# Kernel tuning notes

Hardware: AMD Instinct MI355X
Metric: run time of the kernel (lower is better)

Reference implementation:

```python
import jax, jax.numpy as jnp
import numpy as np
import math

D = 6       # input_size (raw particle features)
H = 128     # hidden_size
B, N, T = 128, 64, 64  # batch, objects, timesteps (T <= max_len 100)


def setup_inputs() -> dict:
    key = jax.random.key(0)
    ks = jax.random.split(key, 16)
    def lin(k, fan_in, shape):
        return (jax.random.uniform(k, shape, jnp.float32) * 2.0 - 1.0) / np.sqrt(fan_in)
    dm = D + H  # 134, PE / readout feature dim
    return {
        "x": jax.random.normal(ks[0], (B, N, T, D), jnp.float32),
        # particle_embedding Linear(D, H)
        "W_emb": lin(ks[1], D, (D, H)), "b_emb": lin(ks[2], D, (H,)),
        # GRU(H, H): torch layout (3H, in)
        "W_ih": lin(ks[3], H, (3 * H, H)), "W_hh": lin(ks[4], H, (3 * H, H)),
        "b_ih": lin(ks[5], H, (3 * H,)), "b_hh": lin(ks[6], H, (3 * H,)),
        # gate_nn: Linear(dm,H) -> SiLU -> Linear(H,1)
        "Wg1": lin(ks[7], dm, (dm, H)), "bg1": lin(ks[8], dm, (H,)),
        "Wg2": lin(ks[9], H, (H, 1)), "bg2": lin(ks[10], H, (1,)),
        # nn: Linear(dm,H) -> SiLU -> Linear(H,H)
        "Wn1": lin(ks[11], dm, (dm, H)), "bn1": lin(ks[12], dm, (H,)),
        "Wn2": lin(ks[13], H, (H, H)), "bn2": lin(ks[14], H, (H,)),
    }


def _positional_encoding(seq_len, d_model, dtype):
    pos = jnp.arange(seq_len, dtype=dtype)[:, None]                      # [T,1]
    div = jnp.exp(jnp.arange(0, d_model, 2, dtype=dtype) * (-math.log(10000.0) / d_model))
    ang = pos * div                                                       # [T, dm/2]
    # interleave sin (even idx) and cos (odd idx)
    return jnp.stack([jnp.sin(ang), jnp.cos(ang)], axis=-1).reshape(seq_len, d_model)


def _gru_last_hidden(y, W_ih, W_hh, b_ih, b_hh):
    # y: [BN, T, H]; PyTorch GRU gate order: r, z, n
    BN, Tn, Hh = y.shape
    xp = y @ W_ih.T + b_ih                       # [BN, T, 3H], input projections
    def step(h, xp_t):
        gh = h @ W_hh.T + b_hh                   # [BN, 3H]
        xr, xz, xn = jnp.split(xp_t, 3, axis=-1)
        hr, hz, hn = jnp.split(gh, 3, axis=-1)
        r = jax.nn.sigmoid(xr + hr)
        z = jax.nn.sigmoid(xz + hz)
        n = jnp.tanh(xn + r * hn)
        h_new = (1.0 - z) * n + z * h
        return h_new, None
    h0 = jnp.zeros((BN, Hh), y.dtype)
    h_last, _ = jax.lax.scan(step, h0, jnp.swapaxes(xp, 0, 1))
    return h_last                                 # [BN, H]


def reference(x, W_emb, b_emb, W_ih, W_hh, b_ih, b_hh,
              Wg1, bg1, Wg2, bg2, Wn1, bn1, Wn2, bn2):
    Bb, Nn, Tt, Dd = x.shape
    Hh = W_emb.shape[1]
    dm = Dd + Hh
    # particle embedding + GRU over time per (batch, object)
    y = (x @ W_emb + b_emb).reshape(Bb * Nn, Tt, Hh)
    h = _gru_last_hidden(y, W_ih, W_hh, b_ih, b_hh)       # [B*N, H]
    # broadcast last hidden state over timesteps, concat with raw positions
    h_exp = jnp.broadcast_to(h[:, None, :], (Bb * Nn, Tt, Hh))
    aug = jnp.concatenate([x.reshape(Bb * Nn, Tt, Dd), h_exp], axis=-1)  # [B*N, T, dm]
    aug = aug + _positional_encoding(Tt, dm, x.dtype)      # PE (dropout in eval = identity)
    feats = aug.reshape(Bb * Nn * Tt, dm)                  # [M, dm]
    # AttentionalAggregation: segment softmax over batch index
    seg = jnp.repeat(jnp.arange(Bb), Nn * Tt)              # [M]
    gate = jax.nn.silu(feats @ Wg1 + bg1) @ Wg2 + bg2      # [M, 1]
    gate = gate[:, 0]
    val = jax.nn.silu(feats @ Wn1 + bn1) @ Wn2 + bn2       # [M, H]
    gmax = jax.ops.segment_max(gate, seg, num_segments=Bb)
    e = jnp.exp(gate - gmax[seg])
    denom = jax.ops.segment_sum(e, seg, num_segments=Bb)
    w = e / denom[seg]                                      # [M]
    out = jax.ops.segment_sum(w[:, None] * val, seg, num_segments=Bb)  # [B, H]
    return out
```

## Files before the change

### kernel.cpp

```cpp
#include <hip/hip_runtime.h>

using bf8v = __bf16 __attribute__((ext_vector_type(8)));
using s4v  = short  __attribute__((ext_vector_type(4)));
using f4v  = float  __attribute__((ext_vector_type(4)));

#define L2E 1.44269504088896340f

__device__ __forceinline__ float ex2(float x){ float r; asm("v_exp_f32 %0, %1" : "=v"(r) : "v"(x)); return r; }
__device__ __forceinline__ float rcp_(float x){ float r; asm("v_rcp_f32 %0, %1" : "=v"(r) : "v"(x)); return r; }
__device__ __forceinline__ float sigm(float x){ return rcp_(1.0f + ex2(-L2E*x)); }
__device__ __forceinline__ float tanh_(float x){ return 1.0f - 2.0f*rcp_(1.0f + ex2(2.0f*L2E*x)); }
__device__ __forceinline__ short f2bf(float x){ return __builtin_bit_cast(short, (__bf16)x); }
__device__ __forceinline__ f4v splat4(float v){ f4v r = {v,v,v,v}; return r; }
__device__ __forceinline__ f4v mfma16(bf8v a, bf8v b, f4v c){
  return __builtin_amdgcn_mfma_f32_16x16x32_bf16(a, b, c, 0, 0, 0);
}

__global__ void prep_kernel(
    const float* __restrict__ W_emb, const float* __restrict__ b_emb,
    const float* __restrict__ W_ih,  const float* __restrict__ W_hh,
    const float* __restrict__ b_ih,
    const float* __restrict__ Wg1,   const float* __restrict__ Wn1,
    const float* __restrict__ Wn2,
    const float* __restrict__ bg1,   const float* __restrict__ bn1,
    short* __restrict__ bhhf, short* __restrict__ wcf, short* __restrict__ wn2f,
    short* __restrict__ w2f, float* __restrict__ b2, float* __restrict__ pe,
    float* __restrict__ bc)
{
  int i = blockIdx.x*256 + threadIdx.x;
  if (i < 49152){
    int e = i&7, lane=(i>>3)&63, r=i>>9; int nt=r%24, kb=r/24;
    int k = kb*32 + ((lane>>4)<<3) + e;
    int n = nt*16 + (lane&15);
    bhhf[i] = f2bf(W_hh[n*128 + k]);
    return;
  }
  i -= 49152;
  if (i < 40960){
    int e=i&7, lane=(i>>3)&63, r=i>>9; int nt=r%16, kb=r/16;
    int k = kb*32 + ((lane>>4)<<3) + e; int n = nt*16 + (lane&15);
    float v = 0.f;
    if (k < 134) v = (n < 128) ? Wg1[k*128 + n] : Wn1[k*128 + (n-128)];
    wcf[i] = f2bf(v);
    return;
  }
  i -= 40960;
  if (i < 16384){
    int e=i&7, lane=(i>>3)&63, r=i>>9; int nt=r%8, kb=r/8;
    int k = kb*32 + ((lane>>4)<<3) + e; int n = nt*16 + (lane&15);
    wn2f[i] = f2bf(Wn2[k*128 + n]);
    return;
  }
  i -= 16384;
  if (i < 12288){
    int e=i&7, lane=(i>>3)&63, nt=i>>9;
    int k = ((lane>>4)<<3) + e; int n = nt*16 + (lane&15);
    float v = 0.f;
    if (k < 6){
      const float* we = W_emb + k*128; const float* wi = W_ih + n*128;
      float s = 0.f;
      for (int h2=0; h2<128; ++h2) s += we[h2]*wi[h2];
      v = s;
    }
    w2f[i] = f2bf(v);
    return;
  }
  i -= 12288;
  if (i < 384){
    float s = b_ih[i]; const float* wi = W_ih + i*128;
    for (int h2=0; h2<128; ++h2) s += b_emb[h2]*wi[h2];
    b2[i] = s;
    return;
  }
  i -= 384;
  if (i < 10240){
    int t = i/160, k = i%160;
    float v = 0.f;
    if (k < 134){
      float fr = expf(-(float)(k & ~1) * 9.210340371976184f / 134.f);
      float a = (float)t * fr;
      v = (k&1) ? cosf(a) : sinf(a);
    }
    pe[i] = v;
    return;
  }
  i -= 10240;
  if (i < 256){ bc[i] = (i < 128) ? bg1[i] : bn1[i-128]; return; }
}

__global__ __launch_bounds__(512, 2) void gru_kernel(
    const float* __restrict__ x,
    const short* __restrict__ bhhf,
    const short* __restrict__ w2f,
    const float* __restrict__ b2,
    const float* __restrict__ b_hh,
    float* __restrict__ h_out)
{
  __shared__ alignas(16) short h_lds[2][16*128];
  const int tid = threadIdx.x;
  const int w = tid >> 6;
  const int lane = tid & 63;
  const int l15 = lane & 15, lhi = lane >> 4;
  const int blk = blockIdx.x;

  for (int i = tid; i < 16*128; i += 512) h_lds[0][i] = 0;

  bf8v bhh[4][3]; bf8v w2v[3];
  float b2v[3], bhv[3];
  #pragma unroll
  for (int g = 0; g < 3; ++g){
    int nt = g*8 + w;
    w2v[g] = *reinterpret_cast<const bf8v*>(w2f + ((nt*64 + lane)<<3));
    #pragma unroll
    for (int kb = 0; kb < 4; ++kb)
      bhh[kb][g] = *reinterpret_cast<const bf8v*>(bhhf + (((kb*24 + nt)*64 + lane)<<3));
    int col = nt*16 + l15;
    b2v[g] = b2[col]; bhv[g] = b_hh[col];
  }
  float hreg[4] = {0.f,0.f,0.f,0.f};
  __syncthreads();

  const float* xrow = x + (size_t)((blk*16 + l15)*64)*6;
  const int sw_r = (l15 & 7) << 4;

  float xv[6];
  #pragma unroll
  for (int j = 0; j < 6; ++j) xv[j] = xrow[j];

#define GSTEP(RD, WR, TN)                                                     \
  {                                                                           \
    bf8v ax;                                                                  \
    _Pragma("unroll")                                                         \
    for (int i2=0;i2<8;++i2) ax[i2] = (__bf16)0.f;                            \
    if (lhi == 0){                                                            \
      ax[0]=(__bf16)xv[0]; ax[1]=(__bf16)xv[1]; ax[2]=(__bf16)xv[2];          \
      ax[3]=(__bf16)xv[3]; ax[4]=(__bf16)xv[4]; ax[5]=(__bf16)xv[5];          \
    }                                                                         \
    float xn[6];                                                              \
    _Pragma("unroll")                                                         \
    for (int j2=0;j2<6;++j2) xn[j2] = xrow[(TN)*6 + j2];                      \
    bf8v ah[4];                                                               \
    _Pragma("unroll")                                                         \
    for (int kb = 0; kb < 4; ++kb){                                           \
      int off = l15*256 + ((kb*64 + lhi*16) ^ sw_r);                          \
      ah[kb] = *reinterpret_cast<const bf8v*>((const char*)(RD) + off);       \
    }                                                                         \
    f4v xpa[3], gha[3];                                                       \
    _Pragma("unroll")                                                         \
    for (int g = 0; g < 3; ++g){                                              \
      xpa[g] = splat4(b2v[g]);                                                \
      xpa[g] = mfma16(ax, w2v[g], xpa[g]);                                    \
      gha[g] = splat4(bhv[g]);                                                \
      _Pragma("unroll")                                                       \
      for (int kb = 0; kb < 4; ++kb) gha[g] = mfma16(ah[kb], bhh[kb][g], gha[g]); \
    }                                                                         \
    _Pragma("unroll")                                                         \
    for (int r = 0; r < 4; ++r){                                              \
      float rg = sigm(xpa[0][r] + gha[0][r]);                                 \
      float zg = sigm(xpa[1][r] + gha[1][r]);                                 \
      float ng = tanh_(xpa[2][r] + rg*gha[2][r]);                             \
      float hv = ng + zg*(hreg[r] - ng);                                      \
      hreg[r] = hv;                                                           \
      int s = lhi*4 + r;                                                      \
      int off = s*256 + (((w*16 + l15)*2) ^ ((s&7)<<4));                      \
      *(short*)((char*)(WR) + off) = f2bf(hv);                                \
    }                                                                         \
    _Pragma("unroll")                                                         \
    for (int j3=0;j3<6;++j3) xv[j3] = xn[j3];                                 \
    __syncthreads();                                                          \
  }

  for (int t = 0; t < 64; t += 2){
    GSTEP(h_lds[0], h_lds[1], t+1);
    GSTEP(h_lds[1], h_lds[0], (t+2 > 63 ? 63 : t+2));
  }
#undef GSTEP

  #pragma unroll
  for (int r = 0; r < 4; ++r){
    int s = lhi*4 + r;
    h_out[(size_t)(blk*16 + s)*128 + w*16 + l15] = hreg[r];
  }
}

__global__ __launch_bounds__(256, 4) void feats_kernel(
    const float* __restrict__ x, const float* __restrict__ h_out,
    const float* __restrict__ pe,
    const short* __restrict__ wcf, const short* __restrict__ wn2f,
    const float* __restrict__ bc, const float* __restrict__ Wg2,
    const float* __restrict__ bg2, const float* __restrict__ bn2,
    float* __restrict__ partials)
{
  __shared__ alignas(16) char AB[64*384];
  __shared__ alignas(16) float hb[160];
  __shared__ alignas(16) float xs[384];
  __shared__ float gp[2][64];
  __shared__ float gate_arr[64];

  const int tid = threadIdx.x;
  const int w = tid >> 6;
  const int lane = tid & 63;
  const int l15 = lane & 15, lhi = lane >> 4;
  const int seq = blockIdx.x;

  if (tid < 160) hb[tid] = (tid >= 6 && tid < 134) ? h_out[(size_t)seq*128 + tid - 6] : 0.f;
  if (tid < 96) *reinterpret_cast<f4v*>(xs + tid*4) =
      *reinterpret_cast<const f4v*>(x + (size_t)seq*384 + tid*4);
  __syncthreads();

  {
    int m = tid >> 2, q = tid & 3, k0 = q*40;
    float xr8[8] = {0.f,0.f,0.f,0.f,0.f,0.f,0.f,0.f};
    if (q == 0){
      #pragma unroll
      for (int j = 0; j < 6; ++j) xr8[j] = xs[m*6 + j];
    }
    const float* per = pe + m*160 + k0;
    const f4v* hb4 = reinterpret_cast<const f4v*>(hb + k0);
    int swm = (m & 7) << 4;
    #pragma unroll
    for (int j = 0; j < 10; ++j){
      f4v v = hb4[j];
      f4v p4 = *reinterpret_cast<const f4v*>(per + 4*j);
      v += p4;
      if (j < 2){
        v[0] += xr8[4*j+0]; v[1] += xr8[4*j+1];
        v[2] += xr8[4*j+2]; v[3] += xr8[4*j+3];
      }
      s4v o;
      #pragma unroll
      for (int c = 0; c < 4; ++c) o[c] = f2bf(v[c]);
      int off = m*384 + (((k0 + 4*j)*2) ^ swm);
      *reinterpret_cast<s4v*>(AB + off) = o;
    }
  }
  __syncthreads();

  const int ntb = w*4;
  float bcv[4];
  #pragma unroll
  for (int i=0;i<4;++i) bcv[i] = bc[(ntb+i)*16 + l15];
  f4v acc[4][4];
  #pragma unroll
  for (int mt=0;mt<4;++mt)
    #pragma unroll
    for (int i=0;i<4;++i) acc[mt][i] = splat4(bcv[i]);
  #pragma unroll
  for (int kb = 0; kb < 5; ++kb){
    bf8v a[4];
    #pragma unroll
    for (int mt=0;mt<4;++mt){
      int row = l15 + 16*mt;
      int off = row*384 + ((kb*64 + lhi*16) ^ ((row&7)<<4));
      a[mt] = *reinterpret_cast<const bf8v*>(AB + off);
    }
    bf8v b[4];
    #pragma unroll
    for (int i=0;i<4;++i)
      b[i] = *reinterpret_cast<const bf8v*>(wcf + (((kb*16 + ntb + i)*64 + lane)<<3));
    #pragma unroll
    for (int mt=0;mt<4;++mt)
      #pragma unroll
      for (int i=0;i<4;++i) acc[mt][i] = mfma16(a[mt], b[i], acc[mt][i]);
  }
  __syncthreads();

  if (w < 2){
    float wg2v[4];
    #pragma unroll
    for (int i=0;i<4;++i) wg2v[i] = Wg2[(ntb+i)*16 + l15];
    #pragma unroll
    for (int mt=0;mt<4;++mt)
      #pragma unroll
      for (int r=0;r<4;++r){
        float p = 0.f;
        #pragma unroll
        for (int i=0;i<4;++i){ float v = acc[mt][i][r]; p += v*sigm(v)*wg2v[i]; }
        p += __shfl_xor(p, 1); p += __shfl_xor(p, 2);
        p += __shfl_xor(p, 4); p += __shfl_xor(p, 8);
        if (l15 == 0) gp[w][mt*16 + lhi*4 + r] = p;
      }
  } else {
    #pragma unroll
    for (int mt=0;mt<4;++mt)
      #pragma unroll
      for (int i=0;i<4;++i)
        #pragma unroll
        for (int r=0;r<4;++r){
          float v = acc[mt][i][r]; float s = v*sigm(v);
          int row = mt*16 + lhi*4 + r;
          int colb = (((w-2)*4 + i)*16 + l15)*2;
          int off = row*256 + (colb ^ ((row&7)<<4));
          *(short*)(AB + off) = f2bf(s);
        }
  }
  __syncthreads();

  if (tid < 64) gate_arr[tid] = bg2[0] + gp[0][tid] + gp[1][tid];

  const int nt2b = w*2;
  float bn2v[2];
  #pragma unroll
  for (int i=0;i<2;++i) bn2v[i] = bn2[(nt2b+i)*16 + l15];
  f4v acc2[4][2];
  #pragma unroll
  for (int mt=0;mt<4;++mt)
    #pragma unroll
    for (int i=0;i<2;++i) acc2[mt][i] = splat4(bn2v[i]);
  #pragma unroll
  for (int kb = 0; kb < 4; ++kb){
    bf8v a2f[4];
    #pragma unroll
    for (int mt=0;mt<4;++mt){
      int row = l15 + 16*mt;
      int off = row*256 + ((kb*64 + lhi*16) ^ ((row&7)<<4));
      a2f[mt] = *reinterpret_cast<const bf8v*>(AB + off);
    }
    bf8v b2f[2];
    #pragma unroll
    for (int i=0;i<2;++i)
      b2f[i] = *reinterpret_cast<const bf8v*>(wn2f + (((kb*8 + nt2b + i)*64 + lane)<<3));
    #pragma unroll
    for (int mt=0;mt<4;++mt)
      #pragma unroll
      for (int i=0;i<2;++i) acc2[mt][i] = mfma16(a2f[mt], b2f[i], acc2[mt][i]);
  }
  __syncthreads();

  float g = gate_arr[lane];
  float M = g;
  #pragma unroll
  for (int d=1; d<64; d<<=1) M = fmaxf(M, __shfl_xor(M, d));
  float e = ex2((g - M)*L2E);
  float sE = e;
  #pragma unroll
  for (int d=1; d<64; d<<=1) sE += __shfl_xor(sE, d);
  float ev0 = 0.f, ev1 = 0.f;
  #pragma unroll
  for (int mt=0;mt<4;++mt)
    #pragma unroll
    for (int r=0;r<4;++r){
      int row = mt*16 + lhi*4 + r;
      float wm = ex2((gate_arr[row] - M)*L2E);
      ev0 += wm*acc2[mt][0][r];
      ev1 += wm*acc2[mt][1][r];
    }
  ev0 += __shfl_xor(ev0, 16); ev0 += __shfl_xor(ev0, 32);
  ev1 += __shfl_xor(ev1, 16); ev1 += __shfl_xor(ev1, 32);

  float* pb = partials + (size_t)seq*130;
  if (tid == 0){ pb[0] = M; pb[1] = sE; }
  if (lane < 16){
    pb[2 + (nt2b+0)*16 + lane] = ev0;
    pb[2 + (nt2b+1)*16 + lane] = ev1;
  }
}

__global__ void combine_kernel(const float* __restrict__ partials, float* __restrict__ out)
{
  int b = blockIdx.x; int j = threadIdx.x;
  const float* pb = partials + (size_t)b*64*130;
  float M = -3.0e38f;
  for (int p = 0; p < 64; ++p) M = fmaxf(M, pb[p*130]);
  float num = 0.f, den = 0.f;
  for (int p = 0; p < 64; ++p){
    float wm = ex2((pb[p*130] - M)*L2E);
    den += wm * pb[p*130 + 1];
    num += wm * pb[p*130 + 2 + j];
  }
  out[b*128 + j] = num / den;
}

extern "C" void kernel_launch(void* const* d_in, const int* in_sizes, int n_in,
                              void* d_out, int out_size, void* d_ws, size_t ws_size,
                              hipStream_t stream) {
  (void)in_sizes; (void)n_in; (void)out_size; (void)ws_size;
  const float* x     = (const float*)d_in[0];
  const float* W_emb = (const float*)d_in[1];
  const float* b_emb = (const float*)d_in[2];
  const float* W_ih  = (const float*)d_in[3];
  const float* W_hh  = (const float*)d_in[4];
  const float* b_ih  = (const float*)d_in[5];
  const float* b_hh  = (const float*)d_in[6];
  const float* Wg1   = (const float*)d_in[7];
  const float* bg1   = (const float*)d_in[8];
  const float* Wg2   = (const float*)d_in[9];
  const float* bg2   = (const float*)d_in[10];
  const float* Wn1   = (const float*)d_in[11];
  const float* bn1   = (const float*)d_in[12];
  const float* Wn2   = (const float*)d_in[13];
  const float* bn2   = (const float*)d_in[14];

  char* p = (char*)d_ws;
  short* bhhf = (short*)p; p += 98304;
  short* wcf  = (short*)p; p += 81920;
  short* wn2f = (short*)p; p += 32768;
  short* w2f  = (short*)p; p += 24576;
  float* b2   = (float*)p; p += 1536;
  float* pe   = (float*)p; p += 40960;
  float* bc   = (float*)p; p += 1024;
  float* h_out    = (float*)p; p += (size_t)8192*128*4;
  float* partials = (float*)p; p += (size_t)8192*130*4;

  prep_kernel<<<507, 256, 0, stream>>>(W_emb, b_emb, W_ih, W_hh, b_ih,
                                       Wg1, Wn1, Wn2, bg1, bn1,
                                       bhhf, wcf, wn2f, w2f, b2, pe, bc);
  gru_kernel<<<512, 512, 0, stream>>>(x, bhhf, w2f, b2, b_hh, h_out);
  feats_kernel<<<8192, 256, 0, stream>>>(x, h_out, pe, wcf, wn2f, bc, Wg2, bg2, bn2, partials);
  combine_kernel<<<128, 128, 0, stream>>>(partials, (float*)d_out);
}
```

Before: 212.3 us.

## Process two sequence groups per GRU block and pre-pack x into bf16 MFMA fragments

The GRU kernel now handles two 16-row groups per block, interleaving their independent MFMA chains and gate math to hide latency, and halves the grid to 256 blocks. The input x is converted in the prep kernel into bf16 fragments laid out for direct 16-byte loads, replacing the per-step scalar float loads and conversions. The feats kernel shrinks its LDS row stride from 384 to 320 bytes, drops the x staging buffer and raises its occupancy hint to 6. The risks are fewer GRU blocks on a large GPU (256 blocks for many CUs), more register pressure, and an extra prep pass that writes about 8 MB.

```diff
diff --git a/kernel.cpp b/kernel.cpp
--- a/kernel.cpp
+++ b/kernel.cpp
@@ -17,6 +17,7 @@
 }
 
 __global__ void prep_kernel(
+    const float* __restrict__ x,
     const float* __restrict__ W_emb, const float* __restrict__ b_emb,
     const float* __restrict__ W_ih,  const float* __restrict__ W_hh,
     const float* __restrict__ b_ih,
@@ -25,7 +26,7 @@
     const float* __restrict__ bg1,   const float* __restrict__ bn1,
     short* __restrict__ bhhf, short* __restrict__ wcf, short* __restrict__ wn2f,
     short* __restrict__ w2f, float* __restrict__ b2, float* __restrict__ pe,
-    float* __restrict__ bc)
+    float* __restrict__ bc, short* __restrict__ xfrag)
 {
   int i = blockIdx.x*256 + threadIdx.x;
   if (i < 49152){
@@ -86,24 +87,35 @@
   }
   i -= 10240;
   if (i < 256){ bc[i] = (i < 128) ? bg1[i] : bn1[i-128]; return; }
+  i -= 256;
+  if (i < 524288){
+    int r = i & 15, t = (i>>4)&63, grp = i>>10;
+    const float* xr = x + ((size_t)(grp*16 + r)*64 + t)*6;
+    s4v lo, hi;
+    lo[0]=f2bf(xr[0]); lo[1]=f2bf(xr[1]); lo[2]=f2bf(xr[2]); lo[3]=f2bf(xr[3]);
+    hi[0]=f2bf(xr[4]); hi[1]=f2bf(xr[5]); hi[2]=0; hi[3]=0;
+    *reinterpret_cast<s4v*>(xfrag + (size_t)i*8)     = lo;
+    *reinterpret_cast<s4v*>(xfrag + (size_t)i*8 + 4) = hi;
+    return;
+  }
 }
 
 __global__ __launch_bounds__(512, 2) void gru_kernel(
-    const float* __restrict__ x,
+    const short* __restrict__ xfrag,
     const short* __restrict__ bhhf,
     const short* __restrict__ w2f,
     const float* __restrict__ b2,
     const float* __restrict__ b_hh,
     float* __restrict__ h_out)
 {
-  __shared__ alignas(16) short h_lds[2][16*128];
+  __shared__ alignas(16) short h_lds[2][2][16*128];
   const int tid = threadIdx.x;
   const int w = tid >> 6;
   const int lane = tid & 63;
   const int l15 = lane & 15, lhi = lane >> 4;
   const int blk = blockIdx.x;
 
-  for (int i = tid; i < 16*128; i += 512) h_lds[0][i] = 0;
+  for (int i = tid; i < 16*128; i += 512){ h_lds[0][0][i] = 0; h_lds[1][0][i] = 0; }
 
   bf8v bhh[4][3]; bf8v w2v[3];
   float b2v[3], bhv[3];
@@ -117,73 +129,75 @@
     int col = nt*16 + l15;
     b2v[g] = b2[col]; bhv[g] = b_hh[col];
   }
-  float hreg[4] = {0.f,0.f,0.f,0.f};
-  __syncthreads();
-
-  const float* xrow = x + (size_t)((blk*16 + l15)*64)*6;
+  float hr0[4] = {0.f,0.f,0.f,0.f};
+  float hr1[4] = {0.f,0.f,0.f,0.f};
+  __syncthreads();
+
+  const short* xf0 = xfrag + (size_t)(2*blk  )*8192 + l15*8;
+  const short* xf1 = xfrag + (size_t)(2*blk+1)*8192 + l15*8;
   const int sw_r = (l15 & 7) << 4;
 
-  float xv[6];
-  #pragma unroll
-  for (int j = 0; j < 6; ++j) xv[j] = xrow[j];
-
-#define GSTEP(RD, WR, TN)                                                     \
+  bf8v ax0 = *reinterpret_cast<const bf8v*>(xf0);
+  bf8v ax1 = *reinterpret_cast<const bf8v*>(xf1);
+
+#define GSTEP(P, T)                                                           \
   {                                                                           \
-    bf8v ax;                                                                  \
-    _Pragma("unroll")                                                         \
-    for (int i2=0;i2<8;++i2) ax[i2] = (__bf16)0.f;                            \
-    if (lhi == 0){                                                            \
-      ax[0]=(__bf16)xv[0]; ax[1]=(__bf16)xv[1]; ax[2]=(__bf16)xv[2];          \
-      ax[3]=(__bf16)xv[3]; ax[4]=(__bf16)xv[4]; ax[5]=(__bf16)xv[5];          \
-    }                                                                         \
-    float xn[6];                                                              \
-    _Pragma("unroll")                                                         \
-    for (int j2=0;j2<6;++j2) xn[j2] = xrow[(TN)*6 + j2];                      \
-    bf8v ah[4];                                                               \
+    int tn = (T) + 1; if (tn > 63) tn = 63;                                   \
+    bf8v axn0 = *reinterpret_cast<const bf8v*>(xf0 + tn*128);                 \
+    bf8v axn1 = *reinterpret_cast<const bf8v*>(xf1 + tn*128);                 \
+    bf8v ah0[4], ah1[4];                                                      \
     _Pragma("unroll")                                                         \
     for (int kb = 0; kb < 4; ++kb){                                           \
       int off = l15*256 + ((kb*64 + lhi*16) ^ sw_r);                          \
-      ah[kb] = *reinterpret_cast<const bf8v*>((const char*)(RD) + off);       \
+      ah0[kb] = *reinterpret_cast<const bf8v*>((const char*)h_lds[0][P] + off); \
+      ah1[kb] = *reinterpret_cast<const bf8v*>((const char*)h_lds[1][P] + off); \
     }                                                                         \
-    f4v xpa[3], gha[3];                                                       \
+    f4v xg0[3], gh0[3], xg1[3], gh1[3];                                       \
     _Pragma("unroll")                                                         \
     for (int g = 0; g < 3; ++g){                                              \
-      xpa[g] = splat4(b2v[g]);                                                \
-      xpa[g] = mfma16(ax, w2v[g], xpa[g]);                                    \
-      gha[g] = splat4(bhv[g]);                                                \
+      xg0[g] = splat4(b2v[g]); xg0[g] = mfma16(ax0, w2v[g], xg0[g]);          \
+      xg1[g] = splat4(b2v[g]); xg1[g] = mfma16(ax1, w2v[g], xg1[g]);          \
+      gh0[g] = splat4(bhv[g]); gh1[g] = splat4(bhv[g]);                       \
       _Pragma("unroll")                                                       \
-      for (int kb = 0; kb < 4; ++kb) gha[g] = mfma16(ah[kb], bhh[kb][g], gha[g]); \
+      for (int kb = 0; kb < 4; ++kb){                                         \
+        gh0[g] = mfma16(ah0[kb], bhh[kb][g], gh0[g]);                         \
+        gh1[g] = mfma16(ah1[kb], bhh[kb][g], gh1[g]);                         \
+      }                                                                       \
     }                                                                         \
     _Pragma("unroll")                                                         \
     for (int r = 0; r < 4; ++r){                                              \
-      float rg = sigm(xpa[0][r] + gha[0][r]);                                 \
-      float zg = sigm(xpa[1][r] + gha[1][r]);                                 \
-      float ng = tanh_(xpa[2][r] + rg*gha[2][r]);                             \
-      float hv = ng + zg*(hreg[r] - ng);                                      \
-      hreg[r] = hv;                                                           \
       int s = lhi*4 + r;                                                      \
-      int off = s*256 + (((w*16 + l15)*2) ^ ((s&7)<<4));                      \
-      *(short*)((char*)(WR) + off) = f2bf(hv);                                \
+      int woff = s*256 + (((w*16 + l15)*2) ^ ((s&7)<<4));                     \
+      { float rg = sigm(xg0[0][r] + gh0[0][r]);                               \
+        float zg = sigm(xg0[1][r] + gh0[1][r]);                               \
+        float ng = tanh_(xg0[2][r] + rg*gh0[2][r]);                           \
+        float hv = ng + zg*(hr0[r] - ng); hr0[r] = hv;                        \
+        *(short*)((char*)h_lds[0][P^1] + woff) = f2bf(hv); }                  \
+      { float rg = sigm(xg1[0][r] + gh1[0][r]);                               \
+        float zg = sigm(xg1[1][r] + gh1[1][r]);                               \
+        float ng = tanh_(xg1[2][r] + rg*gh1[2][r]);                           \
+        float hv = ng + zg*(hr1[r] - ng); hr1[r] = hv;                        \
+        *(short*)((char*)h_lds[1][P^1] + woff) = f2bf(hv); }                  \
     }                                                                         \
-    _Pragma("unroll")                                                         \
-    for (int j3=0;j3<6;++j3) xv[j3] = xn[j3];                                 \
+    ax0 = axn0; ax1 = axn1;                                                   \
     __syncthreads();                                                          \
   }
 
-  for (int t = 0; t < 64; t += 2){
-    GSTEP(h_lds[0], h_lds[1], t+1);
-    GSTEP(h_lds[1], h_lds[0], (t+2 > 63 ? 63 : t+2));
+  for (int tt = 0; tt < 32; ++tt){
+    GSTEP(0, 2*tt);
+    GSTEP(1, 2*tt + 1);
   }
 #undef GSTEP
 
   #pragma unroll
   for (int r = 0; r < 4; ++r){
     int s = lhi*4 + r;
-    h_out[(size_t)(blk*16 + s)*128 + w*16 + l15] = hreg[r];
-  }
-}
-
-__global__ __launch_bounds__(256, 4) void feats_kernel(
+    h_out[(size_t)((2*blk  )*16 + s)*128 + w*16 + l15] = hr0[r];
+    h_out[(size_t)((2*blk+1)*16 + s)*128 + w*16 + l15] = hr1[r];
+  }
+}
+
+__global__ __launch_bounds__(256, 6) void feats_kernel(
     const float* __restrict__ x, const float* __restrict__ h_out,
     const float* __restrict__ pe,
     const short* __restrict__ wcf, const short* __restrict__ wn2f,
@@ -191,9 +205,8 @@
     const float* __restrict__ bg2, const float* __restrict__ bn2,
     float* __restrict__ partials)
 {
-  __shared__ alignas(16) char AB[64*384];
+  __shared__ alignas(16) char AB[64*320];
   __shared__ alignas(16) float hb[160];
-  __shared__ alignas(16) float xs[384];
   __shared__ float gp[2][64];
   __shared__ float gate_arr[64];
 
@@ -204,20 +217,19 @@
   const int seq = blockIdx.x;
 
   if (tid < 160) hb[tid] = (tid >= 6 && tid < 134) ? h_out[(size_t)seq*128 + tid - 6] : 0.f;
-  if (tid < 96) *reinterpret_cast<f4v*>(xs + tid*4) =
-      *reinterpret_cast<const f4v*>(x + (size_t)seq*384 + tid*4);
   __syncthreads();
 
   {
     int m = tid >> 2, q = tid & 3, k0 = q*40;
     float xr8[8] = {0.f,0.f,0.f,0.f,0.f,0.f,0.f,0.f};
     if (q == 0){
-      #pragma unroll
-      for (int j = 0; j < 6; ++j) xr8[j] = xs[m*6 + j];
+      const float* xr = x + (size_t)(seq*64 + m)*6;
+      #pragma unroll
+      for (int j = 0; j < 6; ++j) xr8[j] = xr[j];
     }
     const float* per = pe + m*160 + k0;
     const f4v* hb4 = reinterpret_cast<const f4v*>(hb + k0);
-    int swm = (m & 7) << 4;
+    int swm = (m & 3) << 4;
     #pragma unroll
     for (int j = 0; j < 10; ++j){
       f4v v = hb4[j];
@@ -230,7 +242,7 @@
       s4v o;
       #pragma unroll
       for (int c = 0; c < 4; ++c) o[c] = f2bf(v[c]);
-      int off = m*384 + (((k0 + 4*j)*2) ^ swm);
+      int off = m*320 + (((k0 + 4*j)*2) ^ swm);
       *reinterpret_cast<s4v*>(AB + off) = o;
     }
   }
@@ -251,7 +263,7 @@
     #pragma unroll
     for (int mt=0;mt<4;++mt){
       int row = l15 + 16*mt;
-      int off = row*384 + ((kb*64 + lhi*16) ^ ((row&7)<<4));
+      int off = row*320 + ((kb*64 + lhi*16) ^ ((row&3)<<4));
       a[mt] = *reinterpret_cast<const bf8v*>(AB + off);
     }
     bf8v b[4];
@@ -399,13 +411,14 @@
   float* b2   = (float*)p; p += 1536;
   float* pe   = (float*)p; p += 40960;
   float* bc   = (float*)p; p += 1024;
+  short* xfrag = (short*)p; p += (size_t)524288*8*2;
   float* h_out    = (float*)p; p += (size_t)8192*128*4;
   float* partials = (float*)p; p += (size_t)8192*130*4;
 
-  prep_kernel<<<507, 256, 0, stream>>>(W_emb, b_emb, W_ih, W_hh, b_ih,
-                                       Wg1, Wn1, Wn2, bg1, bn1,
-                                       bhhf, wcf, wn2f, w2f, b2, pe, bc);
-  gru_kernel<<<512, 512, 0, stream>>>(x, bhhf, w2f, b2, b_hh, h_out);
+  prep_kernel<<<2555, 256, 0, stream>>>(x, W_emb, b_emb, W_ih, W_hh, b_ih,
+                                        Wg1, Wn1, Wn2, bg1, bn1,
+                                        bhhf, wcf, wn2f, w2f, b2, pe, bc, xfrag);
+  gru_kernel<<<256, 512, 0, stream>>>(xfrag, bhhf, w2f, b2, b_hh, h_out);
   feats_kernel<<<8192, 256, 0, stream>>>(x, h_out, pe, wcf, wn2f, bc, Wg2, bg2, bn2, partials);
   combine_kernel<<<128, 128, 0, stream>>>(partials, (float*)d_out);
 }
```

New measurement: 353.1 us. +66.3%, slower.
